# Kernel optimization log

Hardware: AMD Instinct MI355X
Metric: run time of the kernel (lower is better)

The kernel has to match this reference:

```python
import jax, jax.numpy as jnp
import numpy as np

DIM = 512
NUM_HEADS = 8
DIM_HEAD = DIM // NUM_HEADS


def _xavier(key, shape):
    fan_in, fan_out = shape[0], shape[1]
    a = (6.0 / (fan_in + fan_out)) ** 0.5
    return jax.random.uniform(key, shape, jnp.float32, -a, a)


def setup_inputs() -> dict:
    key = jax.random.key(0)
    ks = jax.random.split(key, 8)
    B, N, M = 2, 2048, 2048
    x = jax.random.normal(ks[0], (B, N, DIM), jnp.float32)
    source = jax.random.normal(ks[1], (B, M, DIM), jnp.float32)
    source_mask = jax.random.randint(ks[2], (B, M), 0, 2) > 0
    Wq = _xavier(ks[3], (DIM, DIM)); bq = jnp.zeros((DIM,), jnp.float32)
    Wk = _xavier(ks[4], (DIM, DIM)); bk = jnp.zeros((DIM,), jnp.float32)
    Wv = _xavier(ks[5], (DIM, DIM)); bv = jnp.zeros((DIM,), jnp.float32)
    Wm = _xavier(ks[6], (DIM, DIM)); bm = jnp.zeros((DIM,), jnp.float32)
    return {"x": x, "source": source, "source_mask": source_mask,
            "Wq": Wq, "bq": bq, "Wk": Wk, "bk": bk,
            "Wv": Wv, "bv": bv, "Wm": Wm, "bm": bm}


def reference(x, source, source_mask, Wq, bq, Wk, bk, Wv, bv, Wm, bm):
    B, N, D = x.shape
    M = source.shape[-2]
    H, Dh = NUM_HEADS, DIM_HEAD
    # projections (torch Linear: x @ W^T + b)
    q = (x @ Wq.T + bq).reshape(B, N, H, Dh)
    k = (source @ Wk.T + bk).reshape(B, M, H, Dh)
    v = (source @ Wv.T + bv).reshape(B, M, H, Dh)
    scale = 1.0 / (Dh ** 0.5)
    # scores: [B, N, M, H]
    scores = jnp.einsum('bnhd,bmhd->bnmh', q, k) * scale
    scores = jnp.where(source_mask[:, None, :, None], scores, -jnp.inf)
    prob = jax.nn.softmax(scores, axis=-2)  # softmax over m
    agg = jnp.einsum('bnmh,bmhd->bnhd', prob, v).reshape(B, N, D)
    return agg @ Wm.T + bm
```

## Files before the change

kernel.cpp:

```cpp
#include <hip/hip_runtime.h>
#include <hip/hip_bf16.h>

#define DIMF 512
#define NHEAD 8
#define DHEAD 64
#define BATCH 2
#define SEQN 2048
#define SEQM 2048
#define FPS 40
#define QSCALE 0.18033688011112042f

typedef unsigned short u16;
typedef __attribute__((ext_vector_type(8))) short bf16x8;
typedef __attribute__((ext_vector_type(4))) float f32x4;

static __device__ __forceinline__ u16 f2bf(float f) {
    unsigned u = __float_as_uint(f);
    u += 0x7FFF + ((u >> 16) & 1);
    return (u16)(u >> 16);
}

static __device__ __forceinline__
void load16(const u16* g, u16* l) {
    __builtin_amdgcn_global_load_lds(
        (const __attribute__((address_space(1))) void*)g,
        (__attribute__((address_space(3))) void*)l,
        16, 0, 0);
}

static __device__ __forceinline__
void permpair(unsigned& a, unsigned& c) {
#if __has_builtin(__builtin_amdgcn_permlane32_swap)
    {
        auto r1 = __builtin_amdgcn_permlane32_swap(a, c, false, false);
        unsigned a1 = r1[0], c1 = r1[1];
        auto r2 = __builtin_amdgcn_permlane16_swap(a1, c1, false, false);
        a = r2[0]; c = r2[1];
    }
#else
    asm("v_permlane32_swap_b32 %0, %1" : "+v"(a), "+v"(c));
    asm("v_permlane16_swap_b32 %0, %1" : "+v"(a), "+v"(c));
#endif
}

static __device__ __forceinline__
bf16x8 t12pack(f32x4 s0, f32x4 s1) {
    float e00 = __builtin_amdgcn_exp2f(s0[0]);
    float e01 = __builtin_amdgcn_exp2f(s0[1]);
    float e02 = __builtin_amdgcn_exp2f(s0[2]);
    float e03 = __builtin_amdgcn_exp2f(s0[3]);
    float e10 = __builtin_amdgcn_exp2f(s1[0]);
    float e11 = __builtin_amdgcn_exp2f(s1[1]);
    float e12 = __builtin_amdgcn_exp2f(s1[2]);
    float e13 = __builtin_amdgcn_exp2f(s1[3]);
    unsigned a0, a1, c0w, c1w;
    asm("v_cvt_pk_bf16_f32 %0, %1, %2" : "=v"(a0)  : "v"(e00), "v"(e01));
    asm("v_cvt_pk_bf16_f32 %0, %1, %2" : "=v"(a1)  : "v"(e02), "v"(e03));
    asm("v_cvt_pk_bf16_f32 %0, %1, %2" : "=v"(c0w) : "v"(e10), "v"(e11));
    asm("v_cvt_pk_bf16_f32 %0, %1, %2" : "=v"(c1w) : "v"(e12), "v"(e13));
    permpair(a0, c0w);
    permpair(a1, c1w);
    union { unsigned u[4]; bf16x8 hv; } pu;
    pu.u[0] = a0; pu.u[1] = a1; pu.u[2] = c0w; pu.u[3] = c1w;
    return pu.hv;
}

#define LDS_BARRIER() do {                                      \
    asm volatile("s_waitcnt lgkmcnt(0)" ::: "memory");          \
    __builtin_amdgcn_s_barrier();                               \
    __builtin_amdgcn_sched_barrier(0);                          \
} while (0)

__global__ __launch_bounds__(256)
void cvt_w(const float* __restrict__ wq, const float* __restrict__ wk,
           const float* __restrict__ wv, const float* __restrict__ wm,
           const int* __restrict__ mask,
           u16* __restrict__ wqb, u16* __restrict__ wkb,
           u16* __restrict__ wvb, u16* __restrict__ wmb,
           u16* __restrict__ maskbf)
{
    int i = (blockIdx.x * 256 + threadIdx.x) * 4;
    if (blockIdx.y == 4) {
        if (i < BATCH * SEQM) {
            int4 m4 = *(const int4*)&mask[i];
            *(ushort4*)&maskbf[i] = make_ushort4(m4.x ? 0x3F80 : 0, m4.y ? 0x3F80 : 0,
                                                 m4.z ? 0x3F80 : 0, m4.w ? 0x3F80 : 0);
        }
        return;
    }
    const float* in = (blockIdx.y == 0) ? wq : (blockIdx.y == 1) ? wk
                    : (blockIdx.y == 2) ? wv : wm;
    u16* out = (blockIdx.y == 0) ? wqb : (blockIdx.y == 1) ? wkb
             : (blockIdx.y == 2) ? wvb : wmb;
    if (i >= DIMF * DIMF) return;
    float4 v = *(const float4*)&in[i];
    *(ushort4*)&out[i] = make_ushort4(f2bf(v.x), f2bf(v.y), f2bf(v.z), f2bf(v.w));
}

#define ASZ (64 * FPS)
#define BSZ (128 * FPS)

__device__ __forceinline__
void gemm_mfma(const float* __restrict__ Xf, const u16* __restrict__ Xb,
               const u16* __restrict__ W, const float* __restrict__ bias,
               const int* __restrict__ msk, void* __restrict__ Out, int mode)
{
    __shared__ __align__(16) u16 SH[2 * ASZ + 2 * BSZ];

    const int tid  = threadIdx.x;
    const int wave = tid >> 6;
    const int lane = tid & 63;
    const int l15  = lane & 15;
    const int quad = lane >> 4;
    const int wm = wave & 1, wn = wave >> 1;
    const int r0 = blockIdx.x * 64, c0 = blockIdx.y * 128;

    f32x4 acc[2][4] = {};

    const int br = tid >> 2, boct = tid & 3;
    const int ar = tid >> 3, aseg = tid & 7;

    bf16x8 rb0, rb1, rab;
    float4 ra0, ra1;

    auto loadg = [&](int k0) {
        rb0 = *(const bf16x8*)&W[(size_t)(c0 + br) * DIMF + k0 + boct * 8];
        rb1 = *(const bf16x8*)&W[(size_t)(c0 + br + 64) * DIMF + k0 + boct * 8];
        if (Xf) {
            ra0 = *(const float4*)&Xf[(size_t)(r0 + ar) * DIMF + k0 + aseg * 4];
            ra1 = *(const float4*)&Xf[(size_t)(r0 + ar + 32) * DIMF + k0 + aseg * 4];
        } else {
            rab = *(const bf16x8*)&Xb[(size_t)(r0 + br) * DIMF + k0 + boct * 8];
        }
    };
    auto stage = [&](int buf) {
        u16* As = SH + buf * ASZ;
        u16* Bs = SH + 2 * ASZ + buf * BSZ;
        if (Xf) {
            *(ushort4*)&As[ar * FPS + aseg * 4] =
                make_ushort4(f2bf(ra0.x), f2bf(ra0.y), f2bf(ra0.z), f2bf(ra0.w));
            *(ushort4*)&As[(ar + 32) * FPS + aseg * 4] =
                make_ushort4(f2bf(ra1.x), f2bf(ra1.y), f2bf(ra1.z), f2bf(ra1.w));
        } else {
            *(bf16x8*)&As[br * FPS + boct * 8] = rab;
        }
        *(bf16x8*)&Bs[br * FPS + boct * 8] = rb0;
        *(bf16x8*)&Bs[(br + 64) * FPS + boct * 8] = rb1;
    };

    loadg(0);
    stage(0);
    loadg(32);
    LDS_BARRIER();

    const int NK = DIMF / 32;
    for (int kt = 0; kt < NK; ++kt) {
        const int cur = kt & 1;
        if (kt + 1 < NK) stage(cur ^ 1);
        if (kt + 2 < NK) loadg((kt + 2) * 32);
        const u16* As = SH + cur * ASZ;
        const u16* Bs = SH + 2 * ASZ + cur * BSZ;

        bf16x8 af[2], bf[4];
        #pragma unroll
        for (int mi = 0; mi < 2; ++mi)
            af[mi] = *(const bf16x8*)&As[(wm * 32 + mi * 16 + l15) * FPS + quad * 8];
        #pragma unroll
        for (int ni = 0; ni < 4; ++ni)
            bf[ni] = *(const bf16x8*)&Bs[(wn * 64 + ni * 16 + l15) * FPS + quad * 8];
        #pragma unroll
        for (int mi = 0; mi < 2; ++mi)
            #pragma unroll
            for (int ni = 0; ni < 4; ++ni)
                acc[mi][ni] = __builtin_amdgcn_mfma_f32_16x16x32_bf16(
                    af[mi], bf[ni], acc[mi][ni], 0, 0, 0);
        LDS_BARRIER();
    }

    float bb[4];
    #pragma unroll
    for (int ni = 0; ni < 4; ++ni)
        bb[ni] = bias[c0 + wn * 64 + ni * 16 + l15];

    if (mode == 2) {
        u16* T = SH;
        const int b = r0 >> 11;
        const int n_base = r0 & (SEQN - 1);
        #pragma unroll
        for (int hh = 0; hh < 2; ++hh) {
            __syncthreads();
            if (wn == hh) {
                #pragma unroll
                for (int mi = 0; mi < 2; ++mi) {
                    const int rl = wm * 32 + mi * 16 + quad * 4;
                    int4 m4 = *(const int4*)&msk[b * SEQM + n_base + rl];
                    float mm[4];
                    mm[0] = m4.x ? 1.f : 0.f; mm[1] = m4.y ? 1.f : 0.f;
                    mm[2] = m4.z ? 1.f : 0.f; mm[3] = m4.w ? 1.f : 0.f;
                    #pragma unroll
                    for (int ni = 0; ni < 4; ++ni)
                        #pragma unroll
                        for (int r = 0; r < 4; ++r)
                            T[(rl + r) * 72 + ni * 16 + l15] =
                                f2bf((acc[mi][ni][r] + bb[ni]) * mm[r]);
                }
            }
            __syncthreads();
            const int d = tid >> 2, ms = (tid & 3) << 4;
            u16 tmp[16];
            #pragma unroll
            for (int j = 0; j < 16; ++j) tmp[j] = T[(ms + j) * 72 + d];
            const int hgl = (c0 >> 6) + hh;
            u16* dst = (u16*)Out + ((size_t)(b * NHEAD + hgl) * DHEAD + d) * SEQM
                       + n_base + ms;
            *(bf16x8*)&dst[0] = *(bf16x8*)&tmp[0];
            *(bf16x8*)&dst[8] = *(bf16x8*)&tmp[8];
        }
        return;
    }

    #pragma unroll
    for (int mi = 0; mi < 2; ++mi) {
        const int Rbase = r0 + wm * 32 + mi * 16 + quad * 4;
        const int b = Rbase >> 11;
        const int nb = Rbase & (SEQN - 1);
        #pragma unroll
        for (int ni = 0; ni < 4; ++ni) {
            const int C = c0 + wn * 64 + ni * 16 + l15;
            const int h = C >> 6, d = C & 63;
            if (mode == 0) {
                u16* ow = (u16*)Out;
                #pragma unroll
                for (int r = 0; r < 4; ++r)
                    ow[(((size_t)(b * NHEAD + h) * SEQN) + nb + r) * DHEAD + d] =
                        f2bf((acc[mi][ni][r] + bb[ni]) * QSCALE);
            } else if (mode == 1) {
                u16* ow = (u16*)Out;
                #pragma unroll
                for (int r = 0; r < 4; ++r)
                    ow[(((size_t)(b * NHEAD + h) * SEQN) + nb + r) * DHEAD + d] =
                        f2bf(acc[mi][ni][r] + bb[ni]);
            } else {
                float* ow = (float*)Out;
                #pragma unroll
                for (int r = 0; r < 4; ++r)
                    ow[(size_t)(Rbase + r) * DIMF + C] = acc[mi][ni][r] + bb[ni];
            }
        }
    }
}

__global__ __launch_bounds__(256, 3)
void qkv_proj(const float* __restrict__ x, const float* __restrict__ src,
              const u16* __restrict__ wqb, const float* __restrict__ bq,
              const u16* __restrict__ wkb, const float* __restrict__ bk,
              const u16* __restrict__ wvb, const float* __restrict__ bv,
              const int* __restrict__ mask,
              u16* __restrict__ qw, u16* __restrict__ kw, u16* __restrict__ vtw)
{
    const int z = blockIdx.z;
    const float* X = (z == 0) ? x : src;
    const u16* W = (z == 0) ? wqb : (z == 1) ? wkb : wvb;
    const float* B = (z == 0) ? bq : (z == 1) ? bk : bv;
    void* O = (z == 0) ? (void*)qw : (z == 1) ? (void*)kw : (void*)vtw;
    gemm_mfma(X, nullptr, W, B, mask, O, z);
}

__global__ __launch_bounds__(256, 3)
void out_proj(const u16* __restrict__ aggb, const u16* __restrict__ wmb,
              const float* __restrict__ bm, float* __restrict__ out)
{
    gemm_mfma(nullptr, aggb, wmb, bm, nullptr, (void*)out, 3);
}

__global__ __launch_bounds__(256, 2)
void flash_attn_mfma(const u16* __restrict__ q, const u16* __restrict__ k,
                     const u16* __restrict__ vt, const u16* __restrict__ maskbf,
                     u16* __restrict__ agg)
{
    __shared__ __align__(16) u16 KsD[2][8192];
    __shared__ __align__(16) u16 VtsD[2][8192];
    float* Osum = (float*)&KsD[0][0];
    float* Lsum = (float*)&VtsD[0][0];

    const int tid  = threadIdx.x;
    const int wave = tid >> 6;
    const int lane = tid & 63;
    const int l15  = lane & 15;
    const int quad = lane >> 4;
    const int qg = wave >> 1, mh = wave & 1;

    const int bid  = blockIdx.x;
    const int xcd  = bid & 7, slot = bid >> 3;
    const int pair = (xcd << 1) | (slot & 1);
    const int b = pair >> 3, h = pair & 7;
    const int n0 = (slot >> 1) * 64;

    const size_t hoff = (size_t)(b * NHEAD + h) * (size_t)SEQM * DHEAD;
    const u16* kb = k  + hoff;
    const u16* vb = vt + hoff;
    const u16* mb = maskbf + b * SEQM;

    const int dr  = lane >> 3;
    const int kct = (lane & 7) ^ (dr & 7);
    const int vr  = lane >> 4;
    const int vct = (lane & 15) ^ ((4 * wave + vr) & 15);
    const u16* kq[4];
    const u16* vq[4];
    #pragma unroll
    for (int j = 0; j < 4; ++j) {
        const int g = wave + 4 * j;
        kq[j] = kb + (size_t)(g * 8 + dr) * DHEAD + kct * 8;
        vq[j] = vb + (size_t)(g * 4 + vr) * SEQM + vct * 8;
    }

    bf16x8 qf[2][2];
    #pragma unroll
    for (int qh = 0; qh < 2; ++qh) {
        const u16* qp = q + hoff + (size_t)(n0 + qg * 32 + qh * 16 + l15) * DHEAD
                        + quad * 8;
        qf[qh][0] = *(const bf16x8*)qp;
        qf[qh][1] = *(const bf16x8*)(qp + 32);
    }

    #pragma unroll
    for (int j = 0; j < 4; ++j) {
        load16(kq[j], &KsD[0][(wave + 4 * j) * 512]);
        load16(vq[j], &VtsD[0][(wave + 4 * j) * 512]);
    }
    bf16x8 mfA_nxt = *(const bf16x8*)&mb[64 * mh + quad * 8];
    bf16x8 mfB_nxt = *(const bf16x8*)&mb[64 * mh + 32 + quad * 8];

    f32x4 O[2][4] = {};
    f32x4 lacc[2] = {};
    const int NT = SEQM / 128;

    for (int mt = 0; mt < NT; ++mt) {
        const int cur = mt & 1;
        __syncthreads();
        bf16x8 mfA = mfA_nxt, mfB = mfB_nxt;
        if (mt + 1 < NT) {
            const size_t m1 = (size_t)(mt + 1) * 128;
            const int nb = cur ^ 1;
            #pragma unroll
            for (int j = 0; j < 4; ++j) {
                load16(kq[j] + m1 * DHEAD, &KsD[nb][(wave + 4 * j) * 512]);
                load16(vq[j] + m1, &VtsD[nb][(wave + 4 * j) * 512]);
            }
            mfA_nxt = *(const bf16x8*)&mb[m1 + 64 * mh + quad * 8];
            mfB_nxt = *(const bf16x8*)&mb[m1 + 64 * mh + 32 + quad * 8];
        }
        const u16* Ks  = KsD[cur];
        const u16* Vts = VtsD[cur];

        f32x4 st[2][4] = {};
        __builtin_amdgcn_s_setprio(1);
        #pragma unroll
        for (int sub = 0; sub < 4; ++sub) {
            const int mrow = 64 * mh + 16 * sub + l15;
            #pragma unroll
            for (int c = 0; c < 2; ++c) {
                const int oct = (4 * c + quad) ^ (l15 & 7);
                bf16x8 af = *(const bf16x8*)&Ks[mrow * 64 + oct * 8];
                #pragma unroll
                for (int qh = 0; qh < 2; ++qh)
                    st[qh][sub] = __builtin_amdgcn_mfma_f32_16x16x32_bf16(
                        af, qf[qh][c], st[qh][sub], 0, 0, 0);
            }
        }
        __builtin_amdgcn_s_setprio(0);

        bf16x8 pfrA[2], pfrB[2];
        #pragma unroll
        for (int qh = 0; qh < 2; ++qh) {
            pfrA[qh] = t12pack(st[qh][0], st[qh][1]);
            pfrB[qh] = t12pack(st[qh][2], st[qh][3]);
        }

        __builtin_amdgcn_s_setprio(1);
        #pragma unroll
        for (int qh = 0; qh < 2; ++qh) {
            lacc[qh] = __builtin_amdgcn_mfma_f32_16x16x32_bf16(
                pfrA[qh], mfA, lacc[qh], 0, 0, 0);
            lacc[qh] = __builtin_amdgcn_mfma_f32_16x16x32_bf16(
                pfrB[qh], mfB, lacc[qh], 0, 0, 0);
        }
        #pragma unroll
        for (int sd = 0; sd < 4; ++sd) {
            const int pA = (8 * mh + quad) ^ l15;
            const int pB = (8 * mh + 4 + quad) ^ l15;
            bf16x8 vfA = *(const bf16x8*)&Vts[(16 * sd + l15) * 128 + pA * 8];
            bf16x8 vfB = *(const bf16x8*)&Vts[(16 * sd + l15) * 128 + pB * 8];
            #pragma unroll
            for (int qh = 0; qh < 2; ++qh) {
                O[qh][sd] = __builtin_amdgcn_mfma_f32_16x16x32_bf16(
                    pfrA[qh], vfA, O[qh][sd], 0, 0, 0);
                O[qh][sd] = __builtin_amdgcn_mfma_f32_16x16x32_bf16(
                    pfrB[qh], vfB, O[qh][sd], 0, 0, 0);
            }
        }
        __builtin_amdgcn_s_setprio(0);
    }

    __syncthreads();
    if (mh == 1) {
        #pragma unroll
        for (int qh = 0; qh < 2; ++qh) {
            #pragma unroll
            for (int sd = 0; sd < 4; ++sd)
                #pragma unroll
                for (int r = 0; r < 4; ++r)
                    Osum[qg * 2048 + (qh * 16 + quad * 4 + r) * 64 + 16 * sd + l15]
                        = O[qh][sd][r];
            if (l15 == 0) {
                #pragma unroll
                for (int r = 0; r < 4; ++r)
                    Lsum[qg * 32 + qh * 16 + quad * 4 + r] = lacc[qh][r];
            }
        }
    }
    __syncthreads();
    if (mh == 0) {
        #pragma unroll
        for (int qh = 0; qh < 2; ++qh)
            #pragma unroll
            for (int r = 0; r < 4; ++r) {
                const float inv = 1.f /
                    (lacc[qh][r] + Lsum[qg * 32 + qh * 16 + quad * 4 + r]);
                const int n = n0 + qg * 32 + qh * 16 + quad * 4 + r;
                u16* ag = agg + ((size_t)b * SEQN + n) * DIMF + h * DHEAD + l15;
                #pragma unroll
                for (int sd = 0; sd < 4; ++sd)
                    ag[16 * sd] = f2bf((O[qh][sd][r] +
                        Osum[qg * 2048 + (qh * 16 + quad * 4 + r) * 64 + 16 * sd + l15])
                        * inv);
            }
    }
}

extern "C" void kernel_launch(void* const* d_in, const int* in_sizes, int n_in,
                              void* d_out, int out_size, void* d_ws, size_t ws_size,
                              hipStream_t stream)
{
    (void)in_sizes; (void)n_in; (void)out_size; (void)ws_size;
    const float* x      = (const float*)d_in[0];
    const float* source = (const float*)d_in[1];
    const int*   mask   = (const int*)  d_in[2];
    const float* Wq = (const float*)d_in[3]; const float* bq = (const float*)d_in[4];
    const float* Wk = (const float*)d_in[5]; const float* bk = (const float*)d_in[6];
    const float* Wv = (const float*)d_in[7]; const float* bv = (const float*)d_in[8];
    const float* Wm = (const float*)d_in[9]; const float* bm = (const float*)d_in[10];
    float* out = (float*)d_out;

    const size_t SZ = (size_t)BATCH * SEQN * DIMF;
    const size_t WZ = (size_t)DIMF * DIMF;
    u16* qw   = (u16*)d_ws;
    u16* kw   = qw  + SZ;
    u16* vtw  = kw  + SZ;
    u16* aggb = vtw + SZ;
    u16* wqb  = aggb + SZ;
    u16* wkb  = wqb + WZ;
    u16* wvb  = wkb + WZ;
    u16* wmb  = wvb + WZ;
    u16* maskbf = wmb + WZ;

    dim3 gcvt((WZ / 4 + 255) / 256, 5);
    cvt_w<<<gcvt, 256, 0, stream>>>(Wq, Wk, Wv, Wm, mask,
                                    wqb, wkb, wvb, wmb, maskbf);

    dim3 gproj(4096 / 64, 512 / 128, 3);
    qkv_proj<<<gproj, 256, 0, stream>>>(x, source, wqb, bq, wkb, bk, wvb, bv,
                                        mask, qw, kw, vtw);

    flash_attn_mfma<<<512, 256, 0, stream>>>(qw, kw, vtw, maskbf, aggb);

    dim3 gout(4096 / 64, 512 / 128);
    out_proj<<<gout, 256, 0, stream>>>(aggb, wmb, bm, out);
}
```

Before: 137.0 us.

## Load V fragments directly from global memory and raise attention occupancy

Drops the double-buffered LDS staging of the transposed V tile. Each wave now reads its V fragments straight from global memory into registers every iteration, and the launch bound goes from 2 to 3 blocks per CU now that LDS use is halved. This removes the LDS writes and reads for V and is meant to fit more blocks per CU to hide latency. The cost is global or L2 load latency sitting right on the MFMA path with no prefetch, and V is re-read by each wave instead of being shared through LDS.

```diff
diff --git a/kernel.cpp b/kernel.cpp
--- a/kernel.cpp
+++ b/kernel.cpp
@@ -273,15 +273,14 @@
     gemm_mfma(nullptr, aggb, wmb, bm, nullptr, (void*)out, 3);
 }
 
-__global__ __launch_bounds__(256, 2)
+__global__ __launch_bounds__(256, 3)
 void flash_attn_mfma(const u16* __restrict__ q, const u16* __restrict__ k,
                      const u16* __restrict__ vt, const u16* __restrict__ maskbf,
                      u16* __restrict__ agg)
 {
     __shared__ __align__(16) u16 KsD[2][8192];
-    __shared__ __align__(16) u16 VtsD[2][8192];
     float* Osum = (float*)&KsD[0][0];
-    float* Lsum = (float*)&VtsD[0][0];
+    __shared__ float Lsum[64];
 
     const int tid  = threadIdx.x;
     const int wave = tid >> 6;
@@ -303,15 +302,11 @@
 
     const int dr  = lane >> 3;
     const int kct = (lane & 7) ^ (dr & 7);
-    const int vr  = lane >> 4;
-    const int vct = (lane & 15) ^ ((4 * wave + vr) & 15);
     const u16* kq[4];
-    const u16* vq[4];
     #pragma unroll
     for (int j = 0; j < 4; ++j) {
         const int g = wave + 4 * j;
         kq[j] = kb + (size_t)(g * 8 + dr) * DHEAD + kct * 8;
-        vq[j] = vb + (size_t)(g * 4 + vr) * SEQM + vct * 8;
     }
 
     bf16x8 qf[2][2];
@@ -324,16 +319,15 @@
     }
 
     #pragma unroll
-    for (int j = 0; j < 4; ++j) {
+    for (int j = 0; j < 4; ++j)
         load16(kq[j], &KsD[0][(wave + 4 * j) * 512]);
-        load16(vq[j], &VtsD[0][(wave + 4 * j) * 512]);
-    }
     bf16x8 mfA_nxt = *(const bf16x8*)&mb[64 * mh + quad * 8];
     bf16x8 mfB_nxt = *(const bf16x8*)&mb[64 * mh + 32 + quad * 8];
 
     f32x4 O[2][4] = {};
     f32x4 lacc[2] = {};
     const int NT = SEQM / 128;
+    const u16* vw0 = vb + (size_t)l15 * SEQM + 64 * mh + 8 * quad;
 
     for (int mt = 0; mt < NT; ++mt) {
         const int cur = mt & 1;
@@ -343,15 +337,23 @@
             const size_t m1 = (size_t)(mt + 1) * 128;
             const int nb = cur ^ 1;
             #pragma unroll
-            for (int j = 0; j < 4; ++j) {
+            for (int j = 0; j < 4; ++j)
                 load16(kq[j] + m1 * DHEAD, &KsD[nb][(wave + 4 * j) * 512]);
-                load16(vq[j] + m1, &VtsD[nb][(wave + 4 * j) * 512]);
-            }
             mfA_nxt = *(const bf16x8*)&mb[m1 + 64 * mh + quad * 8];
             mfB_nxt = *(const bf16x8*)&mb[m1 + 64 * mh + 32 + quad * 8];
         }
-        const u16* Ks  = KsD[cur];
-        const u16* Vts = VtsD[cur];
+
+        bf16x8 vfA[4], vfB[4];
+        {
+            const u16* vp = vw0 + (size_t)mt * 128;
+            #pragma unroll
+            for (int sd = 0; sd < 4; ++sd) {
+                vfA[sd] = *(const bf16x8*)(vp + (size_t)(16 * sd) * SEQM);
+                vfB[sd] = *(const bf16x8*)(vp + (size_t)(16 * sd) * SEQM + 32);
+            }
+        }
+
+        const u16* Ks = KsD[cur];
 
         f32x4 st[2][4] = {};
         __builtin_amdgcn_s_setprio(1);
@@ -386,19 +388,14 @@
                 pfrB[qh], mfB, lacc[qh], 0, 0, 0);
         }
         #pragma unroll
-        for (int sd = 0; sd < 4; ++sd) {
-            const int pA = (8 * mh + quad) ^ l15;
-            const int pB = (8 * mh + 4 + quad) ^ l15;
-            bf16x8 vfA = *(const bf16x8*)&Vts[(16 * sd + l15) * 128 + pA * 8];
-            bf16x8 vfB = *(const bf16x8*)&Vts[(16 * sd + l15) * 128 + pB * 8];
+        for (int sd = 0; sd < 4; ++sd)
             #pragma unroll
             for (int qh = 0; qh < 2; ++qh) {
                 O[qh][sd] = __builtin_amdgcn_mfma_f32_16x16x32_bf16(
-                    pfrA[qh], vfA, O[qh][sd], 0, 0, 0);
+                    pfrA[qh], vfA[sd], O[qh][sd], 0, 0, 0);
                 O[qh][sd] = __builtin_amdgcn_mfma_f32_16x16x32_bf16(
-                    pfrB[qh], vfB, O[qh][sd], 0, 0, 0);
-            }
-        }
+                    pfrB[qh], vfB[sd], O[qh][sd], 0, 0, 0);
+            }
         __builtin_amdgcn_s_setprio(0);
     }
 
```

Measured after the change: 150.7 us. +9.9%, slower.
